# Optimization experiments

Measured on AMD Instinct MI355X. Metric: run time of the kernel, lower is better.

Reference implementation:

```python
import jax, jax.numpy as jnp
import numpy as np

H = 16
QK_DIM = 1024
EPS = 1e-5


def setup_inputs() -> dict:
    key = jax.random.key(0)
    ks = jax.random.split(key, 5)
    B, N, M, D = 2, 2048, 2048, 1024
    x = jax.random.normal(ks[0], (B, N, D), jnp.float32)
    context = jax.random.normal(ks[1], (B, M, D), jnp.float32)
    Wq = jax.random.normal(ks[2], (QK_DIM, D), jnp.float32) * (D ** -0.5)
    Wkv = jax.random.normal(ks[3], (QK_DIM + 1024, D), jnp.float32) * (D ** -0.5)
    Wtalk = jax.random.normal(ks[4], (H, H), jnp.float32) * (H ** -0.5)
    ln_gamma = jnp.ones((H,), jnp.float32)
    ln_beta = jnp.zeros((H,), jnp.float32)
    return {"x": x, "context": context, "Wq": Wq, "Wkv": Wkv,
            "Wtalk": Wtalk, "ln_gamma": ln_gamma, "ln_beta": ln_beta}


def _split_heads(t):
    # b n (h d) -> b h n d
    b, n, hd = t.shape
    return t.reshape(b, n, H, hd // H).transpose(0, 2, 1, 3)


def reference(x, context, Wq, Wkv, Wtalk, ln_gamma, ln_beta):
    q = x @ Wq.T                      # [B,N,QK]
    kv = context @ Wkv.T              # [B,M,QK+V]
    k, v = kv[..., :QK_DIM], kv[..., QK_DIM:]
    q, k, v = _split_heads(q), _split_heads(k), _split_heads(v)
    q = q * (q.shape[-1] ** -0.5)
    scores = jnp.einsum('bhid,bhjd->bhij', q, k)          # [B,H,N,M]
    aw = jax.nn.softmax(scores, axis=-1)
    # talking heads: Linear over head axis then LayerNorm over head axis
    aw = jnp.einsum('bhij,gh->bgij', aw, Wtalk)
    mu = jnp.mean(aw, axis=1, keepdims=True)
    var = jnp.var(aw, axis=1, keepdims=True)
    aw = (aw - mu) * jax.lax.rsqrt(var + EPS)
    aw = aw * ln_gamma[None, :, None, None] + ln_beta[None, :, None, None]
    attn = jnp.einsum('bhij,bhjd->bhid', aw, v)           # [B,H,N,dv]
    b, h, n, d = attn.shape
    return attn.transpose(0, 2, 1, 3).reshape(b, n, h * d)  # [B,N,V]
```

## Files before the change

kernel.cpp:

```cpp
#include <hip/hip_runtime.h>


typedef __attribute__((ext_vector_type(8))) short short8;
typedef __attribute__((ext_vector_type(4))) short short4v;
typedef __attribute__((ext_vector_type(4))) float float4v;
typedef unsigned short u16;

#define MFMA16(a, b, c) __builtin_amdgcn_mfma_f32_16x16x32_bf16((a), (b), (c), 0, 0, 0)

__device__ inline u16 f2bf(float f) {
  unsigned u = __float_as_uint(f);
  u += 0x7FFFu + ((u >> 16) & 1u);
  return (u16)(u >> 16);
}
__device__ inline float bf2f(u16 u) {
  return __uint_as_float(((unsigned)u) << 16);
}
__device__ inline float fexp2(float x) { return __builtin_amdgcn_exp2f(x); }

__global__ __launch_bounds__(256) void cast_bf16(const float* __restrict__ in,
                                                 u16* __restrict__ out, int n) {
  int i = (blockIdx.x * 256 + threadIdx.x) * 8;
  if (i + 8 > n) return;
  float4v f0 = *(const float4v*)(in + i);
  float4v f1 = *(const float4v*)(in + i + 4);
  short8 o;
  o[0] = (short)f2bf(f0[0]); o[1] = (short)f2bf(f0[1]);
  o[2] = (short)f2bf(f0[2]); o[3] = (short)f2bf(f0[3]);
  o[4] = (short)f2bf(f1[0]); o[5] = (short)f2bf(f1[1]);
  o[6] = (short)f2bf(f1[2]); o[7] = (short)f2bf(f1[3]);
  *(short8*)(out + i) = o;
}

template <int MODE>
__global__ __launch_bounds__(256, 4) void gemm_bt(const u16* __restrict__ A,
                                                  const u16* __restrict__ W,
                                                  u16* __restrict__ out0,
                                                  u16* __restrict__ out1) {
  __shared__ u16 As[64][40];
  __shared__ u16 Ws[64][40];
  const int t = threadIdx.x;
  const int wave = t >> 6, l = t & 63, l15 = l & 15, lq = l >> 4;
  const int r0 = blockIdx.x * 64, c0 = blockIdx.y * 64;
  const int srow = t >> 2, sch = t & 3;
  const u16* ag = A + (r0 + srow) * 1024 + sch * 8;
  const u16* wg = W + (c0 + srow) * 1024 + sch * 8;

  float4v acc[4];
#pragma unroll
  for (int i = 0; i < 4; ++i) acc[i] = (float4v){0.f, 0.f, 0.f, 0.f};

  short8 av = *(const short8*)ag;
  short8 wv = *(const short8*)wg;
  for (int kt = 0; kt < 32; ++kt) {
    __syncthreads();
    *(short8*)&As[srow][sch * 8] = av;
    *(short8*)&Ws[srow][sch * 8] = wv;
    __syncthreads();
    if (kt < 31) {
      av = *(const short8*)(ag + (kt + 1) * 32);
      wv = *(const short8*)(wg + (kt + 1) * 32);
    }
    short8 af = *(const short8*)&As[wave * 16 + l15][lq * 8];
#pragma unroll
    for (int fn = 0; fn < 4; ++fn) {
      short8 bf = *(const short8*)&Ws[fn * 16 + l15][lq * 8];
      acc[fn] = MFMA16(af, bf, acc[fn]);
    }
  }
#pragma unroll
  for (int fn = 0; fn < 4; ++fn) {
#pragma unroll
    for (int r = 0; r < 4; ++r) {
      int row = r0 + wave * 16 + lq * 4 + r;
      int col = c0 + fn * 16 + l15;
      int b = row >> 11, n = row & 2047;
      float v = acc[fn][r];
      if (MODE == 0) {
        v *= 0.125f * 1.44269504088896f;
        int h = col >> 6, d = col & 63;
        out0[(((b * 16 + h) * 2048 + n) << 6) + d] = f2bf(v);
      } else {
        if (col < 1024) {
          int h = col >> 6, d = col & 63;
          out0[(((b * 16 + h) * 2048 + n) << 6) + d] = f2bf(v);
        } else {
          int cc = col - 1024;
          int h = cc >> 6, d = cc & 63;
          out1[(((b * 16 + h) * 2048 + n) << 6) + d] = f2bf(v);
        }
      }
    }
  }
}

__global__ __launch_bounds__(256) void transpose_v(const u16* __restrict__ vh,
                                                   u16* __restrict__ vt) {
  __shared__ u16 tile[64][72];
  const int t = threadIdx.x;
  const int j0 = blockIdx.x * 64, h = blockIdx.y, b = blockIdx.z;
  const u16* src = vh + (((b * 16 + h) * 2048 + j0) << 6);
  int row = t >> 2, c = t & 3;
  short8 v0 = *(const short8*)(src + row * 64 + c * 8);
  short8 v1 = *(const short8*)(src + row * 64 + (c + 4) * 8);
  *(short8*)&tile[row][c * 8] = v0;
  *(short8*)&tile[row][(c + 4) * 8] = v1;
  __syncthreads();
  int d = t >> 2, jc = t & 3;
  short8 o0, o1;
#pragma unroll
  for (int jj = 0; jj < 8; ++jj) o0[jj] = (short)tile[jc * 16 + jj][d];
#pragma unroll
  for (int jj = 0; jj < 8; ++jj) o1[jj] = (short)tile[jc * 16 + 8 + jj][d];
  u16* dst = vt + ((b * 16 + h) * 64 + d) * 2048 + j0 + jc * 16;
  *(short8*)dst = o0;
  *(short8*)(dst + 8) = o1;
}

__global__ __launch_bounds__(256) void qk_exp(const u16* __restrict__ qh,
                                              const u16* __restrict__ kh,
                                              u16* __restrict__ E,
                                              float* __restrict__ lsum,
                                              int i_base) {
  const int t = threadIdx.x;
  const int w = t >> 6, l = t & 63, l15 = l & 15, lq = l >> 4;
  const int it = blockIdx.x;
  const int jt = blockIdx.y;
  const int bh = blockIdx.z;
  const int i0w = it * 64 + w * 16;
  const int ig = i_base + i0w;
  const int j0 = jt * 64;

  const u16* qb = qh + (size_t)(bh * 2048 + ig + l15) * 64 + lq * 8;
  short8 qf0 = *(const short8*)qb;
  short8 qf1 = *(const short8*)(qb + 32);
  const u16* kb = kh + (size_t)(bh * 2048 + j0 + l15) * 64 + lq * 8;

  float4v s[4];
#pragma unroll
  for (int fn = 0; fn < 4; ++fn) {
    short8 k0 = *(const short8*)(kb + fn * 16 * 64);
    short8 k1 = *(const short8*)(kb + fn * 16 * 64 + 32);
    float4v a = {0.f, 0.f, 0.f, 0.f};
    a = MFMA16(k0, qf0, a);
    a = MFMA16(k1, qf1, a);
    s[fn] = a;
  }

  u16* eb = E + ((size_t)(bh * 512 + i0w + l15)) * 2048 + j0 + lq * 4;
  float rs = 0.f;
#pragma unroll
  for (int fn = 0; fn < 4; ++fn) {
    short4v pk;
#pragma unroll
    for (int r = 0; r < 4; ++r) {
      u16 ev = f2bf(fexp2(s[fn][r]));
      pk[r] = (short)ev;
      rs += bf2f(ev);
    }
    *(short4v*)(eb + fn * 16) = pk;
  }
  rs += __shfl_xor(rs, 16);
  rs += __shfl_xor(rs, 32);
  if (l < 16) atomicAdd(lsum + (size_t)bh * 2048 + ig + (l - l15) + l15, rs);
}

__global__ __launch_bounds__(256) void talk_ln(u16* ey,
                                               const float* __restrict__ lsum,
                                               const float* __restrict__ wtalk,
                                               const float* __restrict__ gamma,
                                               const float* __restrict__ beta,
                                               int i_base) {
  __shared__ float wt[256];
  __shared__ float invl[16], ga[16], be[16];
  const int tid = threadIdx.x;
  const int jc = blockIdx.x, iq = blockIdx.y, b = blockIdx.z;
  const int ig = i_base + iq;
  wt[tid] = wtalk[tid];
  if (tid < 16) {
    invl[tid] = 1.f / lsum[(size_t)(b * 16 + tid) * 2048 + ig];
    ga[tid] = gamma[tid];
    be[tid] = beta[tid];
  }
  __syncthreads();

  const int j = jc * 512 + tid * 2;
  const size_t base = ((size_t)(b * 16) * 512 + iq) * 2048 + j;
  const size_t hstride = (size_t)512 * 2048;

  float p0[16], p1[16];
#pragma unroll
  for (int h = 0; h < 16; ++h) {
    unsigned u = *(const unsigned*)(ey + base + h * hstride);
    float il = invl[h];
    p0[h] = bf2f((u16)(u & 0xffffu)) * il;
    p1[h] = bf2f((u16)(u >> 16)) * il;
  }
  float t0[16], t1[16];
#pragma unroll
  for (int g = 0; g < 16; ++g) { t0[g] = 0.f; t1[g] = 0.f; }
#pragma unroll
  for (int h = 0; h < 16; ++h) {
#pragma unroll
    for (int g = 0; g < 16; ++g) {
      float wv = wt[g * 16 + h];
      t0[g] += wv * p0[h];
      t1[g] += wv * p1[h];
    }
  }
  float mu0 = 0.f, mu1 = 0.f, ss0 = 0.f, ss1 = 0.f;
#pragma unroll
  for (int g = 0; g < 16; ++g) {
    mu0 += t0[g]; ss0 += t0[g] * t0[g];
    mu1 += t1[g]; ss1 += t1[g] * t1[g];
  }
  mu0 *= 0.0625f; mu1 *= 0.0625f;
  float rv0 = rsqrtf(ss0 * 0.0625f - mu0 * mu0 + 1e-5f);
  float rv1 = rsqrtf(ss1 * 0.0625f - mu1 * mu1 + 1e-5f);
#pragma unroll
  for (int g = 0; g < 16; ++g) {
    float y0 = (t0[g] - mu0) * rv0 * ga[g] + be[g];
    float y1 = (t1[g] - mu1) * rv1 * ga[g] + be[g];
    unsigned o = (unsigned)f2bf(y0) | ((unsigned)f2bf(y1) << 16);
    *(unsigned*)(ey + base + g * hstride) = o;
  }
}

__global__ __launch_bounds__(256, 4) void pv_gemm(const u16* __restrict__ Y,
                                                  const u16* __restrict__ VT,
                                                  float* __restrict__ out,
                                                  int i_base) {
  __shared__ u16 As[64][40];
  __shared__ u16 Ws[64][40];
  const int t = threadIdx.x;
  const int wave = t >> 6, l = t & 63, l15 = l & 15, lq = l >> 4;
  const int r0 = blockIdx.x * 64;
  const int bg = blockIdx.y;
  const int srow = t >> 2, sch = t & 3;
  const u16* ag = Y + ((size_t)bg * 512 + r0 + srow) * 2048 + sch * 8;
  const u16* wg = VT + ((size_t)bg * 64 + srow) * 2048 + sch * 8;

  float4v acc[4];
#pragma unroll
  for (int i = 0; i < 4; ++i) acc[i] = (float4v){0.f, 0.f, 0.f, 0.f};

  short8 av = *(const short8*)ag;
  short8 wv = *(const short8*)wg;
  for (int kt = 0; kt < 64; ++kt) {
    __syncthreads();
    *(short8*)&As[srow][sch * 8] = av;
    *(short8*)&Ws[srow][sch * 8] = wv;
    __syncthreads();
    if (kt < 63) {
      av = *(const short8*)(ag + (kt + 1) * 32);
      wv = *(const short8*)(wg + (kt + 1) * 32);
    }
    short8 af = *(const short8*)&As[wave * 16 + l15][lq * 8];
#pragma unroll
    for (int fn = 0; fn < 4; ++fn) {
      short8 bf = *(const short8*)&Ws[fn * 16 + l15][lq * 8];
      acc[fn] = MFMA16(af, bf, acc[fn]);
    }
  }
  const int b = bg >> 4, g = bg & 15;
#pragma unroll
  for (int fn = 0; fn < 4; ++fn) {
#pragma unroll
    for (int r = 0; r < 4; ++r) {
      int row = i_base + r0 + wave * 16 + lq * 4 + r;
      int col = g * 64 + fn * 16 + l15;
      out[((size_t)b * 2048 + row) * 1024 + col] = acc[fn][r];
    }
  }
}

extern "C" void kernel_launch(void* const* d_in, const int* in_sizes, int n_in,
                              void* d_out, int out_size, void* d_ws,
                              size_t ws_size, hipStream_t stream) {
  const float* x = (const float*)d_in[0];
  const float* ctx = (const float*)d_in[1];
  const float* Wq = (const float*)d_in[2];
  const float* Wkv = (const float*)d_in[3];
  const float* Wtalk = (const float*)d_in[4];
  const float* gam = (const float*)d_in[5];
  const float* bet = (const float*)d_in[6];
  float* out = (float*)d_out;

  u16* ws = (u16*)d_ws;
  u16* qhb = ws;
  u16* khb = ws + 4194304;
  u16* vtb = ws + 8388608;
  float* lsum = (float*)(ws + 12582912);
  u16* scr = ws + 12845056;
  u16* xb = scr;
  u16* cb = scr + 4194304;
  u16* wqb = scr + 8388608;
  u16* wkvb = scr + 9437184;
  u16* vhb = scr + 11534336;
  u16* E = scr;

  hipMemsetAsync(lsum, 0, 65536 * sizeof(float), stream);

  cast_bf16<<<2048, 256, 0, stream>>>(x, xb, 4194304);
  cast_bf16<<<2048, 256, 0, stream>>>(ctx, cb, 4194304);
  cast_bf16<<<512, 256, 0, stream>>>(Wq, wqb, 1048576);
  cast_bf16<<<1024, 256, 0, stream>>>(Wkv, wkvb, 2097152);

  gemm_bt<0><<<dim3(64, 16), 256, 0, stream>>>(xb, wqb, qhb, nullptr);
  gemm_bt<1><<<dim3(64, 32), 256, 0, stream>>>(cb, wkvb, khb, vhb);

  transpose_v<<<dim3(32, 16, 2), 256, 0, stream>>>(vhb, vtb);

  for (int q = 0; q < 4; ++q) {
    int i_base = q * 512;
    qk_exp<<<dim3(8, 32, 32), 256, 0, stream>>>(qhb, khb, E, lsum, i_base);
    talk_ln<<<dim3(4, 512, 2), 256, 0, stream>>>(E, lsum, Wtalk, gam, bet,
                                                 i_base);
    pv_gemm<<<dim3(8, 32), 256, 0, stream>>>(E, vtb, out, i_base);
  }
}
```

Before: 622.2 us.

## Deepen GEMM K-tiles, reuse K fragments in qk_exp, widen talk_ln per thread

The GEMM and PV kernels now stage 64-wide K slices per iteration instead of 32, which halves the number of barrier pairs and issues two MFMAs per load. qk_exp keeps K fragments in registers and loops over four query sub-tiles, so each K load is reused and the grid is a quarter the size. talk_ln handles four columns per thread with 8-byte loads and stores and runs half as many blocks. These changes trade higher register and LDS use, and lower occupancy, for less sync overhead and more data reuse.

```diff
diff --git a/kernel.cpp b/kernel.cpp
--- a/kernel.cpp
+++ b/kernel.cpp
@@ -37,35 +37,42 @@
                                                   const u16* __restrict__ W,
                                                   u16* __restrict__ out0,
                                                   u16* __restrict__ out1) {
-  __shared__ u16 As[64][40];
-  __shared__ u16 Ws[64][40];
+  __shared__ u16 As[64][72];
+  __shared__ u16 Ws[64][72];
   const int t = threadIdx.x;
   const int wave = t >> 6, l = t & 63, l15 = l & 15, lq = l >> 4;
   const int r0 = blockIdx.x * 64, c0 = blockIdx.y * 64;
   const int srow = t >> 2, sch = t & 3;
-  const u16* ag = A + (r0 + srow) * 1024 + sch * 8;
-  const u16* wg = W + (c0 + srow) * 1024 + sch * 8;
+  const u16* ag = A + (r0 + srow) * 1024 + sch * 16;
+  const u16* wg = W + (c0 + srow) * 1024 + sch * 16;
 
   float4v acc[4];
 #pragma unroll
   for (int i = 0; i < 4; ++i) acc[i] = (float4v){0.f, 0.f, 0.f, 0.f};
 
-  short8 av = *(const short8*)ag;
-  short8 wv = *(const short8*)wg;
-  for (int kt = 0; kt < 32; ++kt) {
+  short8 av0 = *(const short8*)ag, av1 = *(const short8*)(ag + 8);
+  short8 wv0 = *(const short8*)wg, wv1 = *(const short8*)(wg + 8);
+  for (int kt = 0; kt < 16; ++kt) {
     __syncthreads();
-    *(short8*)&As[srow][sch * 8] = av;
-    *(short8*)&Ws[srow][sch * 8] = wv;
+    *(short8*)&As[srow][sch * 16] = av0;
+    *(short8*)&As[srow][sch * 16 + 8] = av1;
+    *(short8*)&Ws[srow][sch * 16] = wv0;
+    *(short8*)&Ws[srow][sch * 16 + 8] = wv1;
     __syncthreads();
-    if (kt < 31) {
-      av = *(const short8*)(ag + (kt + 1) * 32);
-      wv = *(const short8*)(wg + (kt + 1) * 32);
-    }
-    short8 af = *(const short8*)&As[wave * 16 + l15][lq * 8];
+    if (kt < 15) {
+      const u16* an = ag + (kt + 1) * 64;
+      const u16* wn = wg + (kt + 1) * 64;
+      av0 = *(const short8*)an; av1 = *(const short8*)(an + 8);
+      wv0 = *(const short8*)wn; wv1 = *(const short8*)(wn + 8);
+    }
+    short8 af0 = *(const short8*)&As[wave * 16 + l15][lq * 8];
+    short8 af1 = *(const short8*)&As[wave * 16 + l15][32 + lq * 8];
 #pragma unroll
     for (int fn = 0; fn < 4; ++fn) {
-      short8 bf = *(const short8*)&Ws[fn * 16 + l15][lq * 8];
-      acc[fn] = MFMA16(af, bf, acc[fn]);
+      short8 bf0 = *(const short8*)&Ws[fn * 16 + l15][lq * 8];
+      short8 bf1 = *(const short8*)&Ws[fn * 16 + l15][32 + lq * 8];
+      acc[fn] = MFMA16(af0, bf0, acc[fn]);
+      acc[fn] = MFMA16(af1, bf1, acc[fn]);
     }
   }
 #pragma unroll
@@ -117,60 +124,66 @@
   *(short8*)(dst + 8) = o1;
 }
 
-__global__ __launch_bounds__(256) void qk_exp(const u16* __restrict__ qh,
-                                              const u16* __restrict__ kh,
-                                              u16* __restrict__ E,
-                                              float* __restrict__ lsum,
-                                              int i_base) {
+__global__ __launch_bounds__(256, 6) void qk_exp(const u16* __restrict__ qh,
+                                                 const u16* __restrict__ kh,
+                                                 u16* __restrict__ E,
+                                                 float* __restrict__ lsum,
+                                                 int i_base) {
   const int t = threadIdx.x;
   const int w = t >> 6, l = t & 63, l15 = l & 15, lq = l >> 4;
-  const int it = blockIdx.x;
-  const int jt = blockIdx.y;
+  const int ib = blockIdx.x;
+  const int jm = blockIdx.y;
   const int bh = blockIdx.z;
-  const int i0w = it * 64 + w * 16;
-  const int ig = i_base + i0w;
-  const int j0 = jt * 64;
-
-  const u16* qb = qh + (size_t)(bh * 2048 + ig + l15) * 64 + lq * 8;
-  short8 qf0 = *(const short8*)qb;
-  short8 qf1 = *(const short8*)(qb + 32);
+  const int j0 = jm * 256 + w * 64;
+
   const u16* kb = kh + (size_t)(bh * 2048 + j0 + l15) * 64 + lq * 8;
-
-  float4v s[4];
-#pragma unroll
-  for (int fn = 0; fn < 4; ++fn) {
-    short8 k0 = *(const short8*)(kb + fn * 16 * 64);
-    short8 k1 = *(const short8*)(kb + fn * 16 * 64 + 32);
-    float4v a = {0.f, 0.f, 0.f, 0.f};
-    a = MFMA16(k0, qf0, a);
-    a = MFMA16(k1, qf1, a);
-    s[fn] = a;
-  }
-
-  u16* eb = E + ((size_t)(bh * 512 + i0w + l15)) * 2048 + j0 + lq * 4;
-  float rs = 0.f;
-#pragma unroll
-  for (int fn = 0; fn < 4; ++fn) {
-    short4v pk;
-#pragma unroll
-    for (int r = 0; r < 4; ++r) {
-      u16 ev = f2bf(fexp2(s[fn][r]));
-      pk[r] = (short)ev;
-      rs += bf2f(ev);
-    }
-    *(short4v*)(eb + fn * 16) = pk;
-  }
-  rs += __shfl_xor(rs, 16);
-  rs += __shfl_xor(rs, 32);
-  if (l < 16) atomicAdd(lsum + (size_t)bh * 2048 + ig + (l - l15) + l15, rs);
-}
-
-__global__ __launch_bounds__(256) void talk_ln(u16* ey,
-                                               const float* __restrict__ lsum,
-                                               const float* __restrict__ wtalk,
-                                               const float* __restrict__ gamma,
-                                               const float* __restrict__ beta,
-                                               int i_base) {
+  short8 k0 = *(const short8*)(kb);
+  short8 k1 = *(const short8*)(kb + 32);
+  short8 k2 = *(const short8*)(kb + 1024);
+  short8 k3 = *(const short8*)(kb + 1024 + 32);
+  short8 k4 = *(const short8*)(kb + 2048);
+  short8 k5 = *(const short8*)(kb + 2048 + 32);
+  short8 k6 = *(const short8*)(kb + 3072);
+  short8 k7 = *(const short8*)(kb + 3072 + 32);
+
+#pragma unroll 1
+  for (int is = 0; is < 4; ++is) {
+    const int i0 = ib * 64 + is * 16;
+    const u16* qb = qh + (size_t)(bh * 2048 + i_base + i0 + l15) * 64 + lq * 8;
+    short8 qf0 = *(const short8*)qb;
+    short8 qf1 = *(const short8*)(qb + 32);
+    float4v s0 = {0.f, 0.f, 0.f, 0.f}, s1 = s0, s2 = s0, s3 = s0;
+    s0 = MFMA16(k0, qf0, s0); s0 = MFMA16(k1, qf1, s0);
+    s1 = MFMA16(k2, qf0, s1); s1 = MFMA16(k3, qf1, s1);
+    s2 = MFMA16(k4, qf0, s2); s2 = MFMA16(k5, qf1, s2);
+    s3 = MFMA16(k6, qf0, s3); s3 = MFMA16(k7, qf1, s3);
+    u16* eb = E + ((size_t)(bh * 512 + i0 + l15)) * 2048 + j0 + lq * 4;
+    float rs = 0.f;
+#pragma unroll
+    for (int fn = 0; fn < 4; ++fn) {
+      float4v sv = fn == 0 ? s0 : fn == 1 ? s1 : fn == 2 ? s2 : s3;
+      short4v pk;
+#pragma unroll
+      for (int r = 0; r < 4; ++r) {
+        u16 ev = f2bf(fexp2(sv[r]));
+        pk[r] = (short)ev;
+        rs += bf2f(ev);
+      }
+      *(short4v*)(eb + fn * 16) = pk;
+    }
+    rs += __shfl_xor(rs, 16);
+    rs += __shfl_xor(rs, 32);
+    if (l < 16)
+      atomicAdd(lsum + (size_t)bh * 2048 + i_base + i0 + l, rs);
+  }
+}
+
+__global__ __launch_bounds__(256, 5) void talk_ln(u16* ey,
+                                                  const float* __restrict__ lsum,
+                                                  const float* __restrict__ wtalk,
+                                                  const float* __restrict__ gamma,
+                                                  const float* __restrict__ beta,
+                                                  int i_base) {
   __shared__ float wt[256];
   __shared__ float invl[16], ga[16], be[16];
   const int tid = threadIdx.x;
@@ -184,45 +197,53 @@
   }
   __syncthreads();
 
-  const int j = jc * 512 + tid * 2;
+  const int j = jc * 1024 + tid * 4;
   const size_t base = ((size_t)(b * 16) * 512 + iq) * 2048 + j;
-  const size_t hstride = (size_t)512 * 2048;
-
-  float p0[16], p1[16];
+  const size_t hs = (size_t)512 * 2048;
+
+  float t0[16], t1[16], t2[16], t3[16];
+#pragma unroll
+  for (int g = 0; g < 16; ++g) { t0[g] = 0.f; t1[g] = 0.f; t2[g] = 0.f; t3[g] = 0.f; }
 #pragma unroll
   for (int h = 0; h < 16; ++h) {
-    unsigned u = *(const unsigned*)(ey + base + h * hstride);
+    short4v e4 = *(const short4v*)(ey + base + h * hs);
     float il = invl[h];
-    p0[h] = bf2f((u16)(u & 0xffffu)) * il;
-    p1[h] = bf2f((u16)(u >> 16)) * il;
-  }
-  float t0[16], t1[16];
-#pragma unroll
-  for (int g = 0; g < 16; ++g) { t0[g] = 0.f; t1[g] = 0.f; }
-#pragma unroll
-  for (int h = 0; h < 16; ++h) {
+    float p0 = bf2f((u16)e4[0]) * il;
+    float p1 = bf2f((u16)e4[1]) * il;
+    float p2 = bf2f((u16)e4[2]) * il;
+    float p3 = bf2f((u16)e4[3]) * il;
 #pragma unroll
     for (int g = 0; g < 16; ++g) {
       float wv = wt[g * 16 + h];
-      t0[g] += wv * p0[h];
-      t1[g] += wv * p1[h];
-    }
-  }
-  float mu0 = 0.f, mu1 = 0.f, ss0 = 0.f, ss1 = 0.f;
+      t0[g] += wv * p0;
+      t1[g] += wv * p1;
+      t2[g] += wv * p2;
+      t3[g] += wv * p3;
+    }
+  }
+  float mu0 = 0.f, mu1 = 0.f, mu2 = 0.f, mu3 = 0.f;
+  float ss0 = 0.f, ss1 = 0.f, ss2 = 0.f, ss3 = 0.f;
 #pragma unroll
   for (int g = 0; g < 16; ++g) {
     mu0 += t0[g]; ss0 += t0[g] * t0[g];
     mu1 += t1[g]; ss1 += t1[g] * t1[g];
-  }
-  mu0 *= 0.0625f; mu1 *= 0.0625f;
+    mu2 += t2[g]; ss2 += t2[g] * t2[g];
+    mu3 += t3[g]; ss3 += t3[g] * t3[g];
+  }
+  mu0 *= 0.0625f; mu1 *= 0.0625f; mu2 *= 0.0625f; mu3 *= 0.0625f;
   float rv0 = rsqrtf(ss0 * 0.0625f - mu0 * mu0 + 1e-5f);
   float rv1 = rsqrtf(ss1 * 0.0625f - mu1 * mu1 + 1e-5f);
+  float rv2 = rsqrtf(ss2 * 0.0625f - mu2 * mu2 + 1e-5f);
+  float rv3 = rsqrtf(ss3 * 0.0625f - mu3 * mu3 + 1e-5f);
 #pragma unroll
   for (int g = 0; g < 16; ++g) {
-    float y0 = (t0[g] - mu0) * rv0 * ga[g] + be[g];
-    float y1 = (t1[g] - mu1) * rv1 * ga[g] + be[g];
-    unsigned o = (unsigned)f2bf(y0) | ((unsigned)f2bf(y1) << 16);
-    *(unsigned*)(ey + base + g * hstride) = o;
+    float ggg = ga[g], bbb = be[g];
+    short4v o;
+    o[0] = (short)f2bf((t0[g] - mu0) * rv0 * ggg + bbb);
+    o[1] = (short)f2bf((t1[g] - mu1) * rv1 * ggg + bbb);
+    o[2] = (short)f2bf((t2[g] - mu2) * rv2 * ggg + bbb);
+    o[3] = (short)f2bf((t3[g] - mu3) * rv3 * ggg + bbb);
+    *(short4v*)(ey + base + g * hs) = o;
   }
 }
 
@@ -230,36 +251,43 @@
                                                   const u16* __restrict__ VT,
                                                   float* __restrict__ out,
                                                   int i_base) {
-  __shared__ u16 As[64][40];
-  __shared__ u16 Ws[64][40];
+  __shared__ u16 As[64][72];
+  __shared__ u16 Ws[64][72];
   const int t = threadIdx.x;
   const int wave = t >> 6, l = t & 63, l15 = l & 15, lq = l >> 4;
   const int r0 = blockIdx.x * 64;
   const int bg = blockIdx.y;
   const int srow = t >> 2, sch = t & 3;
-  const u16* ag = Y + ((size_t)bg * 512 + r0 + srow) * 2048 + sch * 8;
-  const u16* wg = VT + ((size_t)bg * 64 + srow) * 2048 + sch * 8;
+  const u16* ag = Y + ((size_t)bg * 512 + r0 + srow) * 2048 + sch * 16;
+  const u16* wg = VT + ((size_t)bg * 64 + srow) * 2048 + sch * 16;
 
   float4v acc[4];
 #pragma unroll
   for (int i = 0; i < 4; ++i) acc[i] = (float4v){0.f, 0.f, 0.f, 0.f};
 
-  short8 av = *(const short8*)ag;
-  short8 wv = *(const short8*)wg;
-  for (int kt = 0; kt < 64; ++kt) {
+  short8 av0 = *(const short8*)ag, av1 = *(const short8*)(ag + 8);
+  short8 wv0 = *(const short8*)wg, wv1 = *(const short8*)(wg + 8);
+  for (int kt = 0; kt < 32; ++kt) {
     __syncthreads();
-    *(short8*)&As[srow][sch * 8] = av;
-    *(short8*)&Ws[srow][sch * 8] = wv;
+    *(short8*)&As[srow][sch * 16] = av0;
+    *(short8*)&As[srow][sch * 16 + 8] = av1;
+    *(short8*)&Ws[srow][sch * 16] = wv0;
+    *(short8*)&Ws[srow][sch * 16 + 8] = wv1;
     __syncthreads();
-    if (kt < 63) {
-      av = *(const short8*)(ag + (kt + 1) * 32);
-      wv = *(const short8*)(wg + (kt + 1) * 32);
-    }
-    short8 af = *(const short8*)&As[wave * 16 + l15][lq * 8];
+    if (kt < 31) {
+      const u16* an = ag + (kt + 1) * 64;
+      const u16* wn = wg + (kt + 1) * 64;
+      av0 = *(const short8*)an; av1 = *(const short8*)(an + 8);
+      wv0 = *(const short8*)wn; wv1 = *(const short8*)(wn + 8);
+    }
+    short8 af0 = *(const short8*)&As[wave * 16 + l15][lq * 8];
+    short8 af1 = *(const short8*)&As[wave * 16 + l15][32 + lq * 8];
 #pragma unroll
     for (int fn = 0; fn < 4; ++fn) {
-      short8 bf = *(const short8*)&Ws[fn * 16 + l15][lq * 8];
-      acc[fn] = MFMA16(af, bf, acc[fn]);
+      short8 bf0 = *(const short8*)&Ws[fn * 16 + l15][lq * 8];
+      short8 bf1 = *(const short8*)&Ws[fn * 16 + l15][32 + lq * 8];
+      acc[fn] = MFMA16(af0, bf0, acc[fn]);
+      acc[fn] = MFMA16(af1, bf1, acc[fn]);
     }
   }
   const int b = bg >> 4, g = bg & 15;
@@ -313,8 +341,8 @@
 
   for (int q = 0; q < 4; ++q) {
     int i_base = q * 512;
-    qk_exp<<<dim3(8, 32, 32), 256, 0, stream>>>(qhb, khb, E, lsum, i_base);
-    talk_ln<<<dim3(4, 512, 2), 256, 0, stream>>>(E, lsum, Wtalk, gam, bet,
+    qk_exp<<<dim3(8, 8, 32), 256, 0, stream>>>(qhb, khb, E, lsum, i_base);
+    talk_ln<<<dim3(2, 512, 2), 256, 0, stream>>>(E, lsum, Wtalk, gam, bet,
                                                  i_base);
     pv_gemm<<<dim3(8, 32), 256, 0, stream>>>(E, vtb, out, i_base);
   }
```

Result: slower. 871.8 us (+40.1%).
